# Optimization experiments

Hardware: AMD Instinct MI355X
Metric: run time of the kernel (lower is better)

## Reference

```python
import jax, jax.numpy as jnp
import numpy as np
import math

B, S, D = 16, 2048, 128

def setup_inputs() -> dict:
    key = jax.random.key(0)
    k1, k2, k3, k4 = jax.random.split(key, 4)
    query = jax.random.normal(k1, (B, S, D), dtype=jnp.float32)
    key_t = jax.random.normal(k2, (B, S, D), dtype=jnp.float32)
    value = jax.random.normal(k3, (B, S, D), dtype=jnp.float32)
    attn_mask = jax.random.randint(k4, (B, S, S), 0, 2).astype(bool)
    return {"query": query, "key": key_t, "value": value, "attn_mask": attn_mask}

def reference(query, key, value, attn_mask):
    # score = Q K^T / sqrt(d)  -> [B, Sq, Sk]
    scale = 1.0 / math.sqrt(query.shape[-1])
    score = jnp.einsum('bqd,bkd->bqk', query, key) * scale
    # faithful quirk: masked positions are replaced by the VALUE 1e-9 (not -inf)
    mask_score = jnp.where(attn_mask, jnp.float32(1e-9), score)
    # faithful quirk: softmax over dim=1 (the query axis), as in the torch source
    score_matrix = jax.nn.softmax(mask_score, axis=1)
    # output = softmax(scores) @ V  -> [B, Sq, D]
    output = jnp.einsum('bqk,bkd->bqd', score_matrix, value)
    return output
```

## Files before the change

### kernel.cpp

```cpp
#include <hip/hip_runtime.h>
#include <math.h>

#define NB 16
#define SS 2048
#define DQ 128
#define SCALE 0.08838834764831845f

typedef __bf16 bf16x8 __attribute__((ext_vector_type(8)));
typedef unsigned short ushort8_t __attribute__((ext_vector_type(8)));
typedef float floatx4 __attribute__((ext_vector_type(4)));
typedef unsigned long long u64;

__device__ __forceinline__ unsigned short f2bf(float x) {
  unsigned int u = __float_as_uint(x);
  u += 0x7fffu + ((u >> 16) & 1u);
  return (unsigned short)(u >> 16);
}
union FragU { ushort8_t u; bf16x8 b; };
__device__ __forceinline__ bf16x8 ld_frag(const unsigned short* p) {
  FragU t; t.u = *(const ushort8_t*)p; return t.b;
}
__device__ __forceinline__ floatx4 mfma16(bf16x8 a, bf16x8 b, floatx4 c) {
  return __builtin_amdgcn_mfma_f32_16x16x32_bf16(a, b, c, 0, 0, 0);
}

__device__ __forceinline__ void bar_lds() {
  asm volatile("s_waitcnt lgkmcnt(0)\n\ts_barrier" ::: "memory");
}


__global__ void zero_accum(float* __restrict__ O) {
  float* p = O + (size_t)blockIdx.x * SS * DQ + 16 * DQ;
#pragma unroll
  for (int i = 0; i < 8; ++i) p[threadIdx.x + 256 * i] = 0.f;
}

__global__ __launch_bounds__(256) void compress_mask(
    const int* __restrict__ M, u64* __restrict__ Mb)
{
  const int b = blockIdx.x;
  const int q = blockIdx.y * 4 + (threadIdx.x >> 6);
  const int lane = threadIdx.x & 63;

  const int* row = M + ((size_t)b * SS + q) * SS;
  int v[32];
#pragma unroll
  for (int kt = 0; kt < 32; ++kt) v[kt] = row[kt * 64 + lane];

  u64 w = 0;
#pragma unroll
  for (int kt = 0; kt < 32; ++kt) {
    u64 bal = __ballot(v[kt] != 0);
    if (lane == kt) w = bal;
  }
  u64* orow = Mb + ((size_t)b * SS + q) * 32;
  if (lane < 32) orow[lane] = w;
}

__global__ __launch_bounds__(256, 4) void pass1_bits(
    const float* __restrict__ Q, const float* __restrict__ K,
    const u64* __restrict__ Mb, float* __restrict__ O)
{
  const int kt  = blockIdx.x;
  const int k0  = kt * 64;
  const int b   = blockIdx.y;
  const int qc  = blockIdx.z;
  const int tid = threadIdx.x;
  const int w = tid >> 6, lane = tid & 63, l15 = lane & 15, quad = lane >> 4;

  __shared__ unsigned short Kbf[64][136];
  __shared__ unsigned short Qbf[64][136];
  __shared__ float red[4][64];

  const float* Qb = Q + (size_t)b * SS * DQ;
  const float* Kb = K + (size_t)b * SS * DQ;
  const u64*   Mbb = Mb + (size_t)b * SS * 32 + kt;

  const int srow = tid >> 5;
  const int sc4  = (tid & 31) * 4;

#pragma unroll
  for (int r = 0; r < 8; ++r) {
    int row = srow + r * 8;
    float4 v = *(const float4*)(Kb + (size_t)(k0 + row) * DQ + sc4);
    *(ushort4*)&Kbf[row][sc4] = make_ushort4(f2bf(v.x), f2bf(v.y), f2bf(v.z), f2bf(v.w));
  }

  const int qlane = 16 * w + l15;

  float4 qreg[8];
  u64 mw_nxt;
  {
    const int q0 = qc * 512;
#pragma unroll
    for (int r = 0; r < 8; ++r)
      qreg[r] = *(const float4*)(Qb + (size_t)(q0 + srow + r * 8) * DQ + sc4);
    mw_nxt = Mbb[(size_t)(q0 + qlane) * 32];
  }

  float colacc[16];
#pragma unroll
  for (int t = 0; t < 16; ++t) colacc[t] = 0.f;

  for (int qi = 0; qi < 8; ++qi) {
    bar_lds();
    u64 mw = mw_nxt;
#pragma unroll
    for (int r = 0; r < 8; ++r) {
      float4 v = qreg[r];
      *(ushort4*)&Qbf[srow + r * 8][sc4] =
          make_ushort4(f2bf(v.x), f2bf(v.y), f2bf(v.z), f2bf(v.w));
    }
    bar_lds();
    if (qi < 7) {
      const int qn = qc * 512 + (qi + 1) * 64;
#pragma unroll
      for (int r = 0; r < 8; ++r)
        qreg[r] = *(const float4*)(Qb + (size_t)(qn + srow + r * 8) * DQ + sc4);
      mw_nxt = Mbb[(size_t)(qn + qlane) * 32];
    }

    floatx4 acc[4];
#pragma unroll
    for (int i = 0; i < 4; ++i) acc[i] = (floatx4){0.f, 0.f, 0.f, 0.f};
#pragma unroll
    for (int d0 = 0; d0 < DQ; d0 += 32) {
      bf16x8 bq = ld_frag(&Qbf[qlane][d0 + quad * 8]);
#pragma unroll
      for (int i = 0; i < 4; ++i) {
        bf16x8 ak = ld_frag(&Kbf[16 * i + l15][d0 + quad * 8]);
        acc[i] = mfma16(ak, bq, acc[i]);
      }
    }
#pragma unroll
    for (int i = 0; i < 4; ++i) {
#pragma unroll
      for (int r = 0; r < 4; ++r) {
        int m = (int)(mw >> (16 * i + quad * 4 + r)) & 1;
        float s = m ? 1e-9f : acc[i][r] * SCALE;
        colacc[i * 4 + r] += __expf(s);
      }
    }
  }

#pragma unroll
  for (int t = 0; t < 16; ++t) {
    colacc[t] += __shfl_xor(colacc[t], 1, 64);
    colacc[t] += __shfl_xor(colacc[t], 2, 64);
    colacc[t] += __shfl_xor(colacc[t], 4, 64);
    colacc[t] += __shfl_xor(colacc[t], 8, 64);
  }
  if (l15 == 0) {
#pragma unroll
    for (int i = 0; i < 4; ++i)
#pragma unroll
      for (int r = 0; r < 4; ++r)
        red[w][16 * i + quad * 4 + r] = colacc[i * 4 + r];
  }
  bar_lds();
  if (tid < 64) {
    float s = red[0][tid] + red[1][tid] + red[2][tid] + red[3][tid];
    atomicAdd(O + (size_t)b * SS * DQ + 16 * DQ + k0 + tid, s);
  }
}

__global__ void combine_linv(float* __restrict__ O) {
  const int b  = blockIdx.x;
  const int jb = blockIdx.y * 4;
  float* Ob = O + (size_t)b * SS * DQ;
#pragma unroll
  for (int it = 0; it < 8; ++it) {
    int k = threadIdx.x + 256 * it;
    float inv = 1.0f / Ob[16 * DQ + k];
#pragma unroll
    for (int j = 0; j < 4; ++j)
      Ob[(size_t)(64 * (jb + j)) * DQ + k] = inv;
  }
}

__global__ __launch_bounds__(256, 2) void pass2_bits(
    const float* __restrict__ Q, const float* __restrict__ K,
    const float* __restrict__ V, const u64* __restrict__ Mb,
    float* __restrict__ O)
{
  const int b = blockIdx.y, q0 = blockIdx.x * 64;
  const int tid = threadIdx.x;
  const int w = tid >> 6, lane = tid & 63, l15 = lane & 15, quad = lane >> 4;

  __shared__ unsigned short Kbf[64][136];
  __shared__ unsigned short Es[64][72];
  __shared__ unsigned short Wt[128][72];
  __shared__ float Li[SS];

  const float* Qb = Q + (size_t)b * SS * DQ;
  const float* Kb = K + (size_t)b * SS * DQ;
  const float* Vb = V + (size_t)b * SS * DQ;

  const int srow = tid >> 5;
  const int sc4  = (tid & 31) * 4;

  {
    const float* src = O + ((size_t)b * SS + q0) * DQ;
#pragma unroll
    for (int r = 0; r < 2; ++r) {
      int idx = (tid + r * 256) * 4;
      *(float4*)&Li[idx] = *(const float4*)(src + idx);
    }
  }
  FragU qf[4];
  {
    const float* qrow = Qb + (size_t)(q0 + 16 * w + l15) * DQ;
#pragma unroll
    for (int i = 0; i < 4; ++i) {
      float4 a = *(const float4*)(qrow + 32 * i + quad * 8);
      float4 c = *(const float4*)(qrow + 32 * i + quad * 8 + 4);
      qf[i].u = (ushort8_t){f2bf(a.x), f2bf(a.y), f2bf(a.z), f2bf(a.w),
                            f2bf(c.x), f2bf(c.y), f2bf(c.z), f2bf(c.w)};
    }
  }

  floatx4 accO[8];
#pragma unroll
  for (int j = 0; j < 8; ++j) accO[j] = (floatx4){0.f, 0.f, 0.f, 0.f};

  const u64* brow = Mb + (size_t)(b * SS + q0 + 16 * w + l15) * 32;

  float4 kreg[8], vreg[8];
  u64 mw_nxt;
  const int vk2 = (tid >> 5) * 2;
  {
#pragma unroll
    for (int r = 0; r < 8; ++r)
      kreg[r] = *(const float4*)(Kb + (size_t)(srow + r * 8) * DQ + sc4);
#pragma unroll
    for (int r = 0; r < 4; ++r) {
      int k2 = vk2 + r * 16;
      vreg[2 * r]     = *(const float4*)(Vb + (size_t)(k2)     * DQ + sc4);
      vreg[2 * r + 1] = *(const float4*)(Vb + (size_t)(k2 + 1) * DQ + sc4);
    }
    mw_nxt = brow[0];
  }

  for (int k0 = 0; k0 < SS; k0 += 64) {
    bar_lds();
    u64 mw = mw_nxt;

#pragma unroll
    for (int r = 0; r < 8; ++r) {
      float4 v = kreg[r];
      *(ushort4*)&Kbf[srow + r * 8][sc4] =
          make_ushort4(f2bf(v.x), f2bf(v.y), f2bf(v.z), f2bf(v.w));
    }
#pragma unroll
    for (int r = 0; r < 4; ++r) {
      int k2 = vk2 + r * 16;
      float fa[4] = {vreg[2*r].x, vreg[2*r].y, vreg[2*r].z, vreg[2*r].w};
      float fb[4] = {vreg[2*r+1].x, vreg[2*r+1].y, vreg[2*r+1].z, vreg[2*r+1].w};
#pragma unroll
      for (int i = 0; i < 4; ++i) {
        int d  = sc4 + i;
        int kk = k2 ^ ((((unsigned)d >> 2) & 7) << 3);
        *(ushort2*)&Wt[d][kk] = make_ushort2(f2bf(fa[i]), f2bf(fb[i]));
      }
    }
    bar_lds();

    if (k0 + 64 < SS) {
      const int kn = k0 + 64;
#pragma unroll
      for (int r = 0; r < 8; ++r)
        kreg[r] = *(const float4*)(Kb + (size_t)(kn + srow + r * 8) * DQ + sc4);
#pragma unroll
      for (int r = 0; r < 4; ++r) {
        int k2 = vk2 + r * 16;
        vreg[2 * r]     = *(const float4*)(Vb + (size_t)(kn + k2)     * DQ + sc4);
        vreg[2 * r + 1] = *(const float4*)(Vb + (size_t)(kn + k2 + 1) * DQ + sc4);
      }
      mw_nxt = brow[(kn >> 6)];
    }

    floatx4 acc[4];
#pragma unroll
    for (int j = 0; j < 4; ++j) acc[j] = (floatx4){0.f, 0.f, 0.f, 0.f};
#pragma unroll
    for (int i = 0; i < 4; ++i) {
      bf16x8 bq = qf[i].b;
#pragma unroll
      for (int j = 0; j < 4; ++j) {
        bf16x8 ak = ld_frag(&Kbf[16 * j + l15][32 * i + quad * 8]);
        acc[j] = mfma16(ak, bq, acc[j]);
      }
    }
#pragma unroll
    for (int j = 0; j < 4; ++j) {
      float4 liv = *(const float4*)&Li[k0 + 16 * j + quad * 4];
      float lv[4] = {liv.x, liv.y, liv.z, liv.w};
      unsigned short es[4];
#pragma unroll
      for (int r = 0; r < 4; ++r) {
        int m = (int)(mw >> (16 * j + quad * 4 + r)) & 1;
        float s = m ? 1e-9f : acc[j][r] * SCALE;
        es[r] = f2bf(__expf(s) * lv[r]);
      }
      *(ushort4*)&Es[16 * w + l15][16 * j + quad * 4] =
          make_ushort4(es[0], es[1], es[2], es[3]);
    }
#pragma unroll
    for (int c = 0; c < 2; ++c) {
      bf16x8 be = ld_frag(&Es[16 * w + l15][32 * c + quad * 8]);
#pragma unroll
      for (int j = 0; j < 8; ++j) {
        int d  = 16 * j + l15;
        int kk = (32 * c + quad * 8) ^ ((((unsigned)d >> 2) & 7) << 3);
        bf16x8 aw = ld_frag(&Wt[d][kk]);
        accO[j] = mfma16(aw, be, accO[j]);
      }
    }
  }

#pragma unroll
  for (int j = 0; j < 8; ++j) {
    float* op = O + ((size_t)b * SS + q0 + 16 * w + l15) * DQ + 16 * j + quad * 4;
    *(float4*)op = make_float4(accO[j][0], accO[j][1], accO[j][2], accO[j][3]);
  }
}

__global__ __launch_bounds__(256, 4) void pass1_colsum(
    const float* __restrict__ Q, const float* __restrict__ K,
    const int* __restrict__ M, float* __restrict__ O)
{
  const int k0  = blockIdx.x * 64;
  const int b   = blockIdx.y;
  const int qc  = blockIdx.z;
  const int tid = threadIdx.x;
  const int w = tid >> 6, lane = tid & 63, l15 = lane & 15, quad = lane >> 4;

  __shared__ unsigned short Kbf[64][136];
  __shared__ unsigned short Qbf[64][136];
  __shared__ float red[4][64];

  const float* Qb = Q + (size_t)b * SS * DQ;
  const float* Kb = K + (size_t)b * SS * DQ;
  const int*   Mb = M + (size_t)b * SS * SS;

  const int srow = tid >> 5;
  const int sc4  = (tid & 31) * 4;

#pragma unroll
  for (int r = 0; r < 8; ++r) {
    int row = srow + r * 8;
    float4 v = *(const float4*)(Kb + (size_t)(k0 + row) * DQ + sc4);
    *(ushort4*)&Kbf[row][sc4] = make_ushort4(f2bf(v.x), f2bf(v.y), f2bf(v.z), f2bf(v.w));
  }

  const int qlane = 16 * w + l15;

  float4 qreg[8];
  int4 mv_nxt[4];
  {
    const int q0 = qc * 512;
#pragma unroll
    for (int r = 0; r < 8; ++r)
      qreg[r] = *(const float4*)(Qb + (size_t)(q0 + srow + r * 8) * DQ + sc4);
#pragma unroll
    for (int i = 0; i < 4; ++i)
      mv_nxt[i] = *(const int4*)(Mb + (size_t)(q0 + qlane) * SS + k0 + 16 * i + quad * 4);
  }

  float colacc[16];
#pragma unroll
  for (int t = 0; t < 16; ++t) colacc[t] = 0.f;

  for (int qi = 0; qi < 8; ++qi) {
    bar_lds();
    int4 mv[4] = {mv_nxt[0], mv_nxt[1], mv_nxt[2], mv_nxt[3]};
#pragma unroll
    for (int r = 0; r < 8; ++r) {
      float4 v = qreg[r];
      *(ushort4*)&Qbf[srow + r * 8][sc4] =
          make_ushort4(f2bf(v.x), f2bf(v.y), f2bf(v.z), f2bf(v.w));
    }
    bar_lds();
    if (qi < 7) {
      const int qn = qc * 512 + (qi + 1) * 64;
#pragma unroll
      for (int r = 0; r < 8; ++r)
        qreg[r] = *(const float4*)(Qb + (size_t)(qn + srow + r * 8) * DQ + sc4);
#pragma unroll
      for (int i = 0; i < 4; ++i)
        mv_nxt[i] = *(const int4*)(Mb + (size_t)(qn + qlane) * SS + k0 + 16 * i + quad * 4);
    }

    floatx4 acc[4];
#pragma unroll
    for (int i = 0; i < 4; ++i) acc[i] = (floatx4){0.f, 0.f, 0.f, 0.f};
#pragma unroll
    for (int d0 = 0; d0 < DQ; d0 += 32) {
      bf16x8 bq = ld_frag(&Qbf[qlane][d0 + quad * 8]);
#pragma unroll
      for (int i = 0; i < 4; ++i) {
        bf16x8 ak = ld_frag(&Kbf[16 * i + l15][d0 + quad * 8]);
        acc[i] = mfma16(ak, bq, acc[i]);
      }
    }
#pragma unroll
    for (int i = 0; i < 4; ++i) {
      int mm[4] = {mv[i].x, mv[i].y, mv[i].z, mv[i].w};
#pragma unroll
      for (int r = 0; r < 4; ++r) {
        float s = mm[r] ? 1e-9f : acc[i][r] * SCALE;
        colacc[i * 4 + r] += __expf(s);
      }
    }
  }

#pragma unroll
  for (int t = 0; t < 16; ++t) {
    colacc[t] += __shfl_xor(colacc[t], 1, 64);
    colacc[t] += __shfl_xor(colacc[t], 2, 64);
    colacc[t] += __shfl_xor(colacc[t], 4, 64);
    colacc[t] += __shfl_xor(colacc[t], 8, 64);
  }
  if (l15 == 0) {
#pragma unroll
    for (int i = 0; i < 4; ++i)
#pragma unroll
      for (int r = 0; r < 4; ++r)
        red[w][16 * i + quad * 4 + r] = colacc[i * 4 + r];
  }
  bar_lds();
  if (tid < 64) {
    float s = red[0][tid] + red[1][tid] + red[2][tid] + red[3][tid];
    atomicAdd(O + (size_t)b * SS * DQ + 16 * DQ + k0 + tid, s);
  }
}

__global__ __launch_bounds__(256, 2) void pass2_out(
    const float* __restrict__ Q, const float* __restrict__ K,
    const float* __restrict__ V, const int* __restrict__ M,
    float* __restrict__ O)
{
  const int b = blockIdx.y, q0 = blockIdx.x * 64;
  const int tid = threadIdx.x;
  const int w = tid >> 6, lane = tid & 63, l15 = lane & 15, quad = lane >> 4;

  __shared__ unsigned short Kbf[64][136];
  __shared__ unsigned short Es[64][72];
  __shared__ unsigned short Wt[128][72];
  __shared__ float Li[SS];

  const float* Qb = Q + (size_t)b * SS * DQ;
  const float* Kb = K + (size_t)b * SS * DQ;
  const float* Vb = V + (size_t)b * SS * DQ;
  const int*   Mb = M + (size_t)b * SS * SS;

  const int srow = tid >> 5;
  const int sc4  = (tid & 31) * 4;

  {
    const float* src = O + ((size_t)b * SS + q0) * DQ;
#pragma unroll
    for (int r = 0; r < 2; ++r) {
      int idx = (tid + r * 256) * 4;
      *(float4*)&Li[idx] = *(const float4*)(src + idx);
    }
  }
  FragU qf[4];
  {
    const float* qrow = Qb + (size_t)(q0 + 16 * w + l15) * DQ;
#pragma unroll
    for (int i = 0; i < 4; ++i) {
      float4 a = *(const float4*)(qrow + 32 * i + quad * 8);
      float4 c = *(const float4*)(qrow + 32 * i + quad * 8 + 4);
      qf[i].u = (ushort8_t){f2bf(a.x), f2bf(a.y), f2bf(a.z), f2bf(a.w),
                            f2bf(c.x), f2bf(c.y), f2bf(c.z), f2bf(c.w)};
    }
  }

  floatx4 accO[8];
#pragma unroll
  for (int j = 0; j < 8; ++j) accO[j] = (floatx4){0.f, 0.f, 0.f, 0.f};

  const int* mrow = Mb + (size_t)(q0 + 16 * w + l15) * SS;

  float4 kreg[8], vreg[8];
  int4 mv_nxt[4];
  const int vk2 = (tid >> 5) * 2;
  {
#pragma unroll
    for (int r = 0; r < 8; ++r)
      kreg[r] = *(const float4*)(Kb + (size_t)(srow + r * 8) * DQ + sc4);
#pragma unroll
    for (int r = 0; r < 4; ++r) {
      int k2 = vk2 + r * 16;
      vreg[2 * r]     = *(const float4*)(Vb + (size_t)(k2)     * DQ + sc4);
      vreg[2 * r + 1] = *(const float4*)(Vb + (size_t)(k2 + 1) * DQ + sc4);
    }
#pragma unroll
    for (int j = 0; j < 4; ++j)
      mv_nxt[j] = *(const int4*)(mrow + 16 * j + quad * 4);
  }

  for (int k0 = 0; k0 < SS; k0 += 64) {
    bar_lds();
    int4 mv[4] = {mv_nxt[0], mv_nxt[1], mv_nxt[2], mv_nxt[3]};

#pragma unroll
    for (int r = 0; r < 8; ++r) {
      float4 v = kreg[r];
      *(ushort4*)&Kbf[srow + r * 8][sc4] =
          make_ushort4(f2bf(v.x), f2bf(v.y), f2bf(v.z), f2bf(v.w));
    }
#pragma unroll
    for (int r = 0; r < 4; ++r) {
      int k2 = vk2 + r * 16;
      float fa[4] = {vreg[2*r].x, vreg[2*r].y, vreg[2*r].z, vreg[2*r].w};
      float fb[4] = {vreg[2*r+1].x, vreg[2*r+1].y, vreg[2*r+1].z, vreg[2*r+1].w};
#pragma unroll
      for (int i = 0; i < 4; ++i) {
        int d  = sc4 + i;
        int kk = k2 ^ ((((unsigned)d >> 2) & 7) << 3);
        *(ushort2*)&Wt[d][kk] = make_ushort2(f2bf(fa[i]), f2bf(fb[i]));
      }
    }
    bar_lds();

    if (k0 + 64 < SS) {
      const int kn = k0 + 64;
#pragma unroll
      for (int r = 0; r < 8; ++r)
        kreg[r] = *(const float4*)(Kb + (size_t)(kn + srow + r * 8) * DQ + sc4);
#pragma unroll
      for (int r = 0; r < 4; ++r) {
        int k2 = vk2 + r * 16;
        vreg[2 * r]     = *(const float4*)(Vb + (size_t)(kn + k2)     * DQ + sc4);
        vreg[2 * r + 1] = *(const float4*)(Vb + (size_t)(kn + k2 + 1) * DQ + sc4);
      }
#pragma unroll
      for (int j = 0; j < 4; ++j)
        mv_nxt[j] = *(const int4*)(mrow + kn + 16 * j + quad * 4);
    }

    floatx4 acc[4];
#pragma unroll
    for (int j = 0; j < 4; ++j) acc[j] = (floatx4){0.f, 0.f, 0.f, 0.f};
#pragma unroll
    for (int i = 0; i < 4; ++i) {
      bf16x8 bq = qf[i].b;
#pragma unroll
      for (int j = 0; j < 4; ++j) {
        bf16x8 ak = ld_frag(&Kbf[16 * j + l15][32 * i + quad * 8]);
        acc[j] = mfma16(ak, bq, acc[j]);
      }
    }
#pragma unroll
    for (int j = 0; j < 4; ++j) {
      float4 liv = *(const float4*)&Li[k0 + 16 * j + quad * 4];
      float lv[4] = {liv.x, liv.y, liv.z, liv.w};
      int mm[4] = {mv[j].x, mv[j].y, mv[j].z, mv[j].w};
      unsigned short es[4];
#pragma unroll
      for (int r = 0; r < 4; ++r) {
        float s = mm[r] ? 1e-9f : acc[j][r] * SCALE;
        es[r] = f2bf(__expf(s) * lv[r]);
      }
      *(ushort4*)&Es[16 * w + l15][16 * j + quad * 4] =
          make_ushort4(es[0], es[1], es[2], es[3]);
    }
#pragma unroll
    for (int c = 0; c < 2; ++c) {
      bf16x8 be = ld_frag(&Es[16 * w + l15][32 * c + quad * 8]);
#pragma unroll
      for (int j = 0; j < 8; ++j) {
        int d  = 16 * j + l15;
        int kk = (32 * c + quad * 8) ^ ((((unsigned)d >> 2) & 7) << 3);
        bf16x8 aw = ld_frag(&Wt[d][kk]);
        accO[j] = mfma16(aw, be, accO[j]);
      }
    }
  }

#pragma unroll
  for (int j = 0; j < 8; ++j) {
    float* op = O + ((size_t)b * SS + q0 + 16 * w + l15) * DQ + 16 * j + quad * 4;
    *(float4*)op = make_float4(accO[j][0], accO[j][1], accO[j][2], accO[j][3]);
  }
}

extern "C" void kernel_launch(void* const* d_in, const int* in_sizes, int n_in,
                              void* d_out, int out_size, void* d_ws, size_t ws_size,
                              hipStream_t stream) {
  const float* Q = (const float*)d_in[0];
  const float* K = (const float*)d_in[1];
  const float* V = (const float*)d_in[2];
  const int*   M = (const int*)d_in[3];
  float* O = (float*)d_out;

  const size_t bneed = (size_t)NB * SS * 32 * sizeof(u64);

  zero_accum<<<dim3(NB), 256, 0, stream>>>(O);
  if (d_ws != nullptr && ws_size >= bneed) {
    u64* Mb = (u64*)d_ws;
    compress_mask<<<dim3(NB, 512), 256, 0, stream>>>(M, Mb);
    pass1_bits<<<dim3(32, NB, 4), 256, 0, stream>>>(Q, K, Mb, O);
    combine_linv<<<dim3(NB, 8), 256, 0, stream>>>(O);
    pass2_bits<<<dim3(32, NB), 256, 0, stream>>>(Q, K, V, Mb, O);
  } else {
    pass1_colsum<<<dim3(32, NB, 4), 256, 0, stream>>>(Q, K, M, O);
    combine_linv<<<dim3(NB, 8), 256, 0, stream>>>(O);
    pass2_out<<<dim3(32, NB), 256, 0, stream>>>(Q, K, V, M, O);
  }
}
```

Before: 535.2 us.

## Precast Q/K/V to bf16 MFMA-fragment layout in workspace, drop LDS staging

Adds pre-pass kernels that convert Q and K to bf16 in per-lane MFMA fragment order, and V to a transposed bf16 fragment layout, all stored in workspace. Both attention passes then load operand fragments directly from global memory with vector loads. This removes the repeated fp32-to-bf16 conversion, the LDS staging and the barriers inside the main loops. In exchange it adds two extra launches, about three bf16 tensor copies of workspace traffic, and a larger workspace requirement; if the workspace is too small, the fallback path runs instead.

```diff
diff --git a/kernel.cpp b/kernel.cpp
--- a/kernel.cpp
+++ b/kernel.cpp
@@ -57,88 +57,120 @@
   if (lane < 32) orow[lane] = w;
 }
 
-__global__ __launch_bounds__(256, 4) void pass1_bits(
+__global__ __launch_bounds__(256) void cast_qk(
     const float* __restrict__ Q, const float* __restrict__ K,
+    unsigned short* __restrict__ Qf, unsigned short* __restrict__ Kf)
+{
+  const int b = blockIdx.x, t = blockIdx.y;
+  const float* src = (blockIdx.z ? K : Q) + ((size_t)b * SS + t * 64) * DQ;
+  unsigned short* dst = (blockIdx.z ? Kf : Qf) + ((size_t)b * 32 + t) * 8192;
+  const int tid = threadIdx.x;
+  const int w16 = tid >> 6, l15 = (tid >> 2) & 15, quad = tid & 3;
+  const float* row = src + (size_t)(16 * w16 + l15) * DQ;
+#pragma unroll
+  for (int i = 0; i < 4; ++i) {
+    float4 a = *(const float4*)(row + 32 * i + quad * 8);
+    float4 c = *(const float4*)(row + 32 * i + quad * 8 + 4);
+    ushort8_t f = {f2bf(a.x), f2bf(a.y), f2bf(a.z), f2bf(a.w),
+                   f2bf(c.x), f2bf(c.y), f2bf(c.z), f2bf(c.w)};
+    *(ushort8_t*)(dst + (((w16 * 4 + i) * 16 + l15) * 4 + quad) * 8) = f;
+  }
+}
+
+__global__ __launch_bounds__(256, 2) void cast_vt(
+    const float* __restrict__ V, unsigned short* __restrict__ Vtf)
+{
+  const int b = blockIdx.x, t = blockIdx.y;
+  const int tid = threadIdx.x;
+  __shared__ unsigned short Wt[128][72];
+
+  const float* Vb = V + ((size_t)b * SS + t * 64) * DQ;
+  const int vk2 = (tid >> 5) * 2, sc4 = (tid & 31) * 4;
+#pragma unroll
+  for (int r = 0; r < 4; ++r) {
+    int k2 = vk2 + r * 16;
+    float4 a  = *(const float4*)(Vb + (size_t)k2 * DQ + sc4);
+    float4 c2 = *(const float4*)(Vb + (size_t)(k2 + 1) * DQ + sc4);
+    float fa[4] = {a.x, a.y, a.z, a.w};
+    float fb[4] = {c2.x, c2.y, c2.z, c2.w};
+#pragma unroll
+    for (int i = 0; i < 4; ++i) {
+      int d  = sc4 + i;
+      int kk = k2 ^ ((((unsigned)d >> 2) & 7) << 3);
+      *(ushort2*)&Wt[d][kk] = make_ushort2(f2bf(fa[i]), f2bf(fb[i]));
+    }
+  }
+  bar_lds();
+
+  unsigned short* dst = Vtf + ((size_t)b * 32 + t) * 8192;
+#pragma unroll
+  for (int it = 0; it < 4; ++it) {
+    int idx = tid + 256 * it;
+    int j = idx >> 7, c = (idx >> 6) & 1, l15 = (idx >> 2) & 15, quad = idx & 3;
+    int d  = 16 * j + l15;
+    int kk = (32 * c + quad * 8) ^ ((((unsigned)d >> 2) & 7) << 3);
+    *(ushort8_t*)(dst + (size_t)idx * 8) = *(const ushort8_t*)&Wt[d][kk];
+  }
+}
+
+__global__ __launch_bounds__(256, 4) void pass1_frag(
+    const unsigned short* __restrict__ Qf, const unsigned short* __restrict__ Kf,
     const u64* __restrict__ Mb, float* __restrict__ O)
 {
-  const int kt  = blockIdx.x;
-  const int k0  = kt * 64;
-  const int b   = blockIdx.y;
-  const int qc  = blockIdx.z;
+  const int kt = blockIdx.x, b = blockIdx.y, qc = blockIdx.z;
   const int tid = threadIdx.x;
   const int w = tid >> 6, lane = tid & 63, l15 = lane & 15, quad = lane >> 4;
 
-  __shared__ unsigned short Kbf[64][136];
-  __shared__ unsigned short Qbf[64][136];
   __shared__ float red[4][64];
 
-  const float* Qb = Q + (size_t)b * SS * DQ;
-  const float* Kb = K + (size_t)b * SS * DQ;
-  const u64*   Mbb = Mb + (size_t)b * SS * 32 + kt;
-
-  const int srow = tid >> 5;
-  const int sc4  = (tid & 31) * 4;
-
-#pragma unroll
-  for (int r = 0; r < 8; ++r) {
-    int row = srow + r * 8;
-    float4 v = *(const float4*)(Kb + (size_t)(k0 + row) * DQ + sc4);
-    *(ushort4*)&Kbf[row][sc4] = make_ushort4(f2bf(v.x), f2bf(v.y), f2bf(v.z), f2bf(v.w));
-  }
-
-  const int qlane = 16 * w + l15;
-
-  float4 qreg[8];
-  u64 mw_nxt;
-  {
-    const int q0 = qc * 512;
-#pragma unroll
-    for (int r = 0; r < 8; ++r)
-      qreg[r] = *(const float4*)(Qb + (size_t)(q0 + srow + r * 8) * DQ + sc4);
-    mw_nxt = Mbb[(size_t)(q0 + qlane) * 32];
-  }
+  const size_t lq = (size_t)(l15 * 4 + quad) * 8;
+  const unsigned short* kfb = Kf + ((size_t)b * 32 + kt) * 8192 + lq;
+  const u64* Mbb = Mb + (size_t)b * SS * 32 + kt;
 
   float colacc[16];
 #pragma unroll
-  for (int t = 0; t < 16; ++t) colacc[t] = 0.f;
+  for (int i = 0; i < 16; ++i) colacc[i] = 0.f;
+
+  FragU qn[4];
+  u64 mwn;
+  {
+    const int t = qc * 8;
+    const unsigned short* qfb = Qf + ((size_t)(b * 32 + t) * 4 + w) * 2048 + lq;
+#pragma unroll
+    for (int i = 0; i < 4; ++i) qn[i].u = *(const ushort8_t*)(qfb + i * 512);
+    mwn = Mbb[(size_t)(t * 64 + 16 * w + l15) * 32];
+  }
 
   for (int qi = 0; qi < 8; ++qi) {
-    bar_lds();
-    u64 mw = mw_nxt;
-#pragma unroll
-    for (int r = 0; r < 8; ++r) {
-      float4 v = qreg[r];
-      *(ushort4*)&Qbf[srow + r * 8][sc4] =
-          make_ushort4(f2bf(v.x), f2bf(v.y), f2bf(v.z), f2bf(v.w));
-    }
-    bar_lds();
+    FragU qf4[4] = {qn[0], qn[1], qn[2], qn[3]};
+    u64 mw = mwn;
     if (qi < 7) {
-      const int qn = qc * 512 + (qi + 1) * 64;
-#pragma unroll
-      for (int r = 0; r < 8; ++r)
-        qreg[r] = *(const float4*)(Qb + (size_t)(qn + srow + r * 8) * DQ + sc4);
-      mw_nxt = Mbb[(size_t)(qn + qlane) * 32];
+      const int t = qc * 8 + qi + 1;
+      const unsigned short* qfb = Qf + ((size_t)(b * 32 + t) * 4 + w) * 2048 + lq;
+#pragma unroll
+      for (int i = 0; i < 4; ++i) qn[i].u = *(const ushort8_t*)(qfb + i * 512);
+      mwn = Mbb[(size_t)(t * 64 + 16 * w + l15) * 32];
     }
 
     floatx4 acc[4];
 #pragma unroll
-    for (int i = 0; i < 4; ++i) acc[i] = (floatx4){0.f, 0.f, 0.f, 0.f};
-#pragma unroll
-    for (int d0 = 0; d0 < DQ; d0 += 32) {
-      bf16x8 bq = ld_frag(&Qbf[qlane][d0 + quad * 8]);
-#pragma unroll
-      for (int i = 0; i < 4; ++i) {
-        bf16x8 ak = ld_frag(&Kbf[16 * i + l15][d0 + quad * 8]);
-        acc[i] = mfma16(ak, bq, acc[i]);
-      }
-    }
+    for (int s = 0; s < 4; ++s) acc[s] = (floatx4){0.f, 0.f, 0.f, 0.f};
 #pragma unroll
     for (int i = 0; i < 4; ++i) {
+      bf16x8 bq = qf4[i].b;
+#pragma unroll
+      for (int s = 0; s < 4; ++s) {
+        bf16x8 ak = ld_frag(kfb + (s * 4 + i) * 512);
+        acc[s] = mfma16(ak, bq, acc[s]);
+      }
+    }
+#pragma unroll
+    for (int s = 0; s < 4; ++s) {
 #pragma unroll
       for (int r = 0; r < 4; ++r) {
-        int m = (int)(mw >> (16 * i + quad * 4 + r)) & 1;
-        float s = m ? 1e-9f : acc[i][r] * SCALE;
-        colacc[i * 4 + r] += __expf(s);
+        int m = (int)(mw >> (16 * s + quad * 4 + r)) & 1;
+        float sv = m ? 1e-9f : acc[s][r] * SCALE;
+        colacc[s * 4 + r] += __expf(sv);
       }
     }
   }
@@ -152,15 +184,15 @@
   }
   if (l15 == 0) {
 #pragma unroll
-    for (int i = 0; i < 4; ++i)
+    for (int s = 0; s < 4; ++s)
 #pragma unroll
       for (int r = 0; r < 4; ++r)
-        red[w][16 * i + quad * 4 + r] = colacc[i * 4 + r];
+        red[w][16 * s + quad * 4 + r] = colacc[s * 4 + r];
   }
   bar_lds();
   if (tid < 64) {
     float s = red[0][tid] + red[1][tid] + red[2][tid] + red[3][tid];
-    atomicAdd(O + (size_t)b * SS * DQ + 16 * DQ + k0 + tid, s);
+    atomicAdd(O + (size_t)b * SS * DQ + 16 * DQ + kt * 64 + tid, s);
   }
 }
 
@@ -178,26 +210,17 @@
   }
 }
 
-__global__ __launch_bounds__(256, 2) void pass2_bits(
-    const float* __restrict__ Q, const float* __restrict__ K,
-    const float* __restrict__ V, const u64* __restrict__ Mb,
+__global__ __launch_bounds__(256, 2) void pass2_frag(
+    const unsigned short* __restrict__ Qf, const unsigned short* __restrict__ Kf,
+    const unsigned short* __restrict__ Vtf, const u64* __restrict__ Mb,
     float* __restrict__ O)
 {
   const int b = blockIdx.y, q0 = blockIdx.x * 64;
   const int tid = threadIdx.x;
   const int w = tid >> 6, lane = tid & 63, l15 = lane & 15, quad = lane >> 4;
 
-  __shared__ unsigned short Kbf[64][136];
   __shared__ unsigned short Es[64][72];
-  __shared__ unsigned short Wt[128][72];
   __shared__ float Li[SS];
-
-  const float* Qb = Q + (size_t)b * SS * DQ;
-  const float* Kb = K + (size_t)b * SS * DQ;
-  const float* Vb = V + (size_t)b * SS * DQ;
-
-  const int srow = tid >> 5;
-  const int sc4  = (tid & 31) * 4;
 
   {
     const float* src = O + ((size_t)b * SS + q0) * DQ;
@@ -207,87 +230,40 @@
       *(float4*)&Li[idx] = *(const float4*)(src + idx);
     }
   }
-  FragU qf[4];
-  {
-    const float* qrow = Qb + (size_t)(q0 + 16 * w + l15) * DQ;
+
+  const size_t lq = (size_t)(l15 * 4 + quad) * 8;
+  FragU qf4[4];
+  {
+    const unsigned short* qfb =
+        Qf + ((size_t)(b * 32 + (q0 >> 6)) * 4 + w) * 2048 + lq;
+#pragma unroll
+    for (int i = 0; i < 4; ++i) qf4[i].u = *(const ushort8_t*)(qfb + i * 512);
+  }
+  const u64* brow = Mb + (size_t)(b * SS + q0 + 16 * w + l15) * 32;
+
+  floatx4 accO[8];
+#pragma unroll
+  for (int j = 0; j < 8; ++j) accO[j] = (floatx4){0.f, 0.f, 0.f, 0.f};
+
+  bar_lds();
+
+  u64 mwn = brow[0];
+  for (int kt = 0; kt < 32; ++kt) {
+    u64 mw = mwn;
+    if (kt < 31) mwn = brow[kt + 1];
+    const unsigned short* kfb = Kf + ((size_t)b * 32 + kt) * 8192 + lq;
+    const unsigned short* vfb = Vtf + ((size_t)b * 32 + kt) * 8192 + lq;
+    const int k0 = kt * 64;
+
+    floatx4 acc[4];
+#pragma unroll
+    for (int j = 0; j < 4; ++j) acc[j] = (floatx4){0.f, 0.f, 0.f, 0.f};
 #pragma unroll
     for (int i = 0; i < 4; ++i) {
-      float4 a = *(const float4*)(qrow + 32 * i + quad * 8);
-      float4 c = *(const float4*)(qrow + 32 * i + quad * 8 + 4);
-      qf[i].u = (ushort8_t){f2bf(a.x), f2bf(a.y), f2bf(a.z), f2bf(a.w),
-                            f2bf(c.x), f2bf(c.y), f2bf(c.z), f2bf(c.w)};
-    }
-  }
-
-  floatx4 accO[8];
-#pragma unroll
-  for (int j = 0; j < 8; ++j) accO[j] = (floatx4){0.f, 0.f, 0.f, 0.f};
-
-  const u64* brow = Mb + (size_t)(b * SS + q0 + 16 * w + l15) * 32;
-
-  float4 kreg[8], vreg[8];
-  u64 mw_nxt;
-  const int vk2 = (tid >> 5) * 2;
-  {
-#pragma unroll
-    for (int r = 0; r < 8; ++r)
-      kreg[r] = *(const float4*)(Kb + (size_t)(srow + r * 8) * DQ + sc4);
-#pragma unroll
-    for (int r = 0; r < 4; ++r) {
-      int k2 = vk2 + r * 16;
-      vreg[2 * r]     = *(const float4*)(Vb + (size_t)(k2)     * DQ + sc4);
-      vreg[2 * r + 1] = *(const float4*)(Vb + (size_t)(k2 + 1) * DQ + sc4);
-    }
-    mw_nxt = brow[0];
-  }
-
-  for (int k0 = 0; k0 < SS; k0 += 64) {
-    bar_lds();
-    u64 mw = mw_nxt;
-
-#pragma unroll
-    for (int r = 0; r < 8; ++r) {
-      float4 v = kreg[r];
-      *(ushort4*)&Kbf[srow + r * 8][sc4] =
-          make_ushort4(f2bf(v.x), f2bf(v.y), f2bf(v.z), f2bf(v.w));
-    }
-#pragma unroll
-    for (int r = 0; r < 4; ++r) {
-      int k2 = vk2 + r * 16;
-      float fa[4] = {vreg[2*r].x, vreg[2*r].y, vreg[2*r].z, vreg[2*r].w};
-      float fb[4] = {vreg[2*r+1].x, vreg[2*r+1].y, vreg[2*r+1].z, vreg[2*r+1].w};
-#pragma unroll
-      for (int i = 0; i < 4; ++i) {
-        int d  = sc4 + i;
-        int kk = k2 ^ ((((unsigned)d >> 2) & 7) << 3);
-        *(ushort2*)&Wt[d][kk] = make_ushort2(f2bf(fa[i]), f2bf(fb[i]));
-      }
-    }
-    bar_lds();
-
-    if (k0 + 64 < SS) {
-      const int kn = k0 + 64;
-#pragma unroll
-      for (int r = 0; r < 8; ++r)
-        kreg[r] = *(const float4*)(Kb + (size_t)(kn + srow + r * 8) * DQ + sc4);
-#pragma unroll
-      for (int r = 0; r < 4; ++r) {
-        int k2 = vk2 + r * 16;
-        vreg[2 * r]     = *(const float4*)(Vb + (size_t)(kn + k2)     * DQ + sc4);
-        vreg[2 * r + 1] = *(const float4*)(Vb + (size_t)(kn + k2 + 1) * DQ + sc4);
-      }
-      mw_nxt = brow[(kn >> 6)];
-    }
-
-    floatx4 acc[4];
-#pragma unroll
-    for (int j = 0; j < 4; ++j) acc[j] = (floatx4){0.f, 0.f, 0.f, 0.f};
-#pragma unroll
-    for (int i = 0; i < 4; ++i) {
-      bf16x8 bq = qf[i].b;
+      bf16x8 bq = qf4[i].b;
 #pragma unroll
       for (int j = 0; j < 4; ++j) {
-        bf16x8 ak = ld_frag(&Kbf[16 * j + l15][32 * i + quad * 8]);
+        bf16x8 ak = ld_frag(kfb + (j * 4 + i) * 512);
         acc[j] = mfma16(ak, bq, acc[j]);
       }
     }
@@ -299,8 +275,8 @@
 #pragma unroll
       for (int r = 0; r < 4; ++r) {
         int m = (int)(mw >> (16 * j + quad * 4 + r)) & 1;
-        float s = m ? 1e-9f : acc[j][r] * SCALE;
-        es[r] = f2bf(__expf(s) * lv[r]);
+        float sv = m ? 1e-9f : acc[j][r] * SCALE;
+        es[r] = f2bf(__expf(sv) * lv[r]);
       }
       *(ushort4*)&Es[16 * w + l15][16 * j + quad * 4] =
           make_ushort4(es[0], es[1], es[2], es[3]);
@@ -310,9 +286,7 @@
       bf16x8 be = ld_frag(&Es[16 * w + l15][32 * c + quad * 8]);
 #pragma unroll
       for (int j = 0; j < 8; ++j) {
-        int d  = 16 * j + l15;
-        int kk = (32 * c + quad * 8) ^ ((((unsigned)d >> 2) & 7) << 3);
-        bf16x8 aw = ld_frag(&Wt[d][kk]);
+        bf16x8 aw = ld_frag(vfb + (j * 2 + c) * 512);
         accO[j] = mfma16(aw, be, accO[j]);
       }
     }
@@ -596,15 +570,22 @@
   const int*   M = (const int*)d_in[3];
   float* O = (float*)d_out;
 
-  const size_t bneed = (size_t)NB * SS * 32 * sizeof(u64);
+  const size_t msz = (size_t)NB * SS * 32 * sizeof(u64);
+  const size_t fsz = (size_t)NB * SS * DQ * sizeof(unsigned short);
+  const size_t need = msz + 3 * fsz;
 
   zero_accum<<<dim3(NB), 256, 0, stream>>>(O);
-  if (d_ws != nullptr && ws_size >= bneed) {
-    u64* Mb = (u64*)d_ws;
-    compress_mask<<<dim3(NB, 512), 256, 0, stream>>>(M, Mb);
-    pass1_bits<<<dim3(32, NB, 4), 256, 0, stream>>>(Q, K, Mb, O);
+  if (d_ws != nullptr && ws_size >= need) {
+    u64* Mbp = (u64*)d_ws;
+    unsigned short* Qf  = (unsigned short*)((char*)d_ws + msz);
+    unsigned short* Kf  = (unsigned short*)((char*)d_ws + msz + fsz);
+    unsigned short* Vtf = (unsigned short*)((char*)d_ws + msz + 2 * fsz);
+    compress_mask<<<dim3(NB, 512), 256, 0, stream>>>(M, Mbp);
+    cast_qk<<<dim3(NB, 32, 2), 256, 0, stream>>>(Q, K, Qf, Kf);
+    cast_vt<<<dim3(NB, 32), 256, 0, stream>>>(V, Vtf);
+    pass1_frag<<<dim3(32, NB, 4), 256, 0, stream>>>(Qf, Kf, Mbp, O);
     combine_linv<<<dim3(NB, 8), 256, 0, stream>>>(O);
-    pass2_bits<<<dim3(32, NB), 256, 0, stream>>>(Q, K, V, Mb, O);
+    pass2_frag<<<dim3(32, NB), 256, 0, stream>>>(Qf, Kf, Vtf, Mbp, O);
   } else {
     pass1_colsum<<<dim3(32, NB, 4), 256, 0, stream>>>(Q, K, M, O);
     combine_linv<<<dim3(NB, 8), 256, 0, stream>>>(O);
```

Measured after the change: 739.7 us. 38.2% more time.
